# Optimization experiments

Measured on AMD Instinct MI355X. Metric: run time of the kernel, lower is better.

Reference implementation:

```python
import jax, jax.numpy as jnp
import numpy as np

N, D = 8192, 128
TEMPERATURE = 0.5


def _l2_normalize(x, eps):
    # matches F.normalize / utils.sim_matrix norm clamping
    n = jnp.linalg.norm(x, axis=1, keepdims=True)
    return x / jnp.maximum(n, eps)


def setup_inputs() -> dict:
    key = jax.random.key(0)
    k1, k2, k3 = jax.random.split(key, 3)
    nodes = jax.random.normal(k1, (N, D), dtype=jnp.float32)
    pair_nodes = jax.random.normal(k2, (N, D), dtype=jnp.float32)
    nodes_labels = jax.random.randint(k3, (N,), 0, 20).astype(jnp.int64)
    # standard NT-Xent self-mask: exclude diagonal from the denominator
    mask = jnp.eye(N, dtype=bool)
    return {"nodes": nodes, "pair_nodes": pair_nodes,
            "nodes_labels": nodes_labels, "mask": mask}


def reference(nodes, pair_nodes, nodes_labels, mask):
    # z, z_p: F.normalize(..., dim=1), eps=1e-12
    z = _l2_normalize(nodes, 1e-12)
    z_p = _l2_normalize(pair_nodes, 1e-12)
    # pairwise cosine similarity [N, N] == z @ z_p.T since rows are unit-norm
    positive_similarity = jnp.einsum('id,jd->ij', z, z_p)
    nominator = jnp.exp(positive_similarity / TEMPERATURE)  # [N, N]
    # utils.sim_matrix(nodes, nodes): cosine sim matrix with eps=1e-8 clamp
    zn = _l2_normalize(nodes, 1e-8)
    similarity_matrix = jnp.einsum('id,jd->ij', zn, zn)  # [N, N]
    denominator = (~mask).astype(jnp.float32) * jnp.exp(similarity_matrix / TEMPERATURE)
    den_sum = jnp.sum(denominator, axis=1)  # [N]
    # torch broadcasting: [N,N] / [N] divides along the LAST axis (columns)
    loss_partial = -jnp.log(nominator / den_sum[None, :])
    loss = jnp.sum(loss_partial) / nodes.shape[0]
    return loss
```

## Files before the change

kernel.cpp:

```cpp
#include <hip/hip_runtime.h>

#define N 8192
#define D 128
#define EXP_SCALE 2.8853900817779268f

typedef __bf16 bf16;
typedef __bf16 bf16x8 __attribute__((ext_vector_type(8)));
typedef float f32x4 __attribute__((ext_vector_type(4)));

#define ZBF_OFF 0
#define DEN_OFF (N * D * 2)
#define S_OFF   (DEN_OFF + N * 4)
#define SP_OFF  (S_OFF + 512)

__global__ __launch_bounds__(64) void norm_kernel(
    const float* __restrict__ nodes, const float* __restrict__ pair,
    bf16* __restrict__ zbf, float* __restrict__ svec, float* __restrict__ spvec)
{
    const int lane = threadIdx.x;
    const bool isPair = blockIdx.x >= 512;
    const float* src = isPair ? pair : nodes;
    const int row0 = (blockIdx.x & 511) * 16;

    float acc0 = 0.f, acc1 = 0.f;
    for (int rr = 0; rr < 16; ++rr) {
        const int row = row0 + rr;
        const float x0 = src[row * D + lane];
        const float x1 = src[row * D + lane + 64];
        float ss = x0 * x0 + x1 * x1;
        #pragma unroll
        for (int m = 32; m >= 1; m >>= 1) ss += __shfl_xor(ss, m, 64);
        const float nrm = sqrtf(ss);
        const float inv12 = 1.f / fmaxf(nrm, 1e-12f);
        acc0 += x0 * inv12;
        acc1 += x1 * inv12;
        if (!isPair) {
            const float inv8 = 1.f / fmaxf(nrm, 1e-8f);
            zbf[row * D + lane]      = (bf16)(x0 * inv8);
            zbf[row * D + lane + 64] = (bf16)(x1 * inv8);
        }
    }
    float* dst = isPair ? spvec : svec;
    atomicAdd(&dst[lane], acc0);
    atomicAdd(&dst[lane + 64], acc1);
}

#define LDP 80

__global__ __launch_bounds__(256) void gemm_kernel(
    const bf16* __restrict__ zbf, float* __restrict__ den)
{
    __shared__ bf16 As[128 * LDP];
    __shared__ bf16 Bs[128 * LDP];

    const int tid  = threadIdx.x;
    const int lane = tid & 63, wave = tid >> 6;
    const int wm = wave >> 1, wn = wave & 1;
    const int quad = lane >> 4, c = lane & 15;
    const int jbase = blockIdx.y * 128;
    const int kbase = blockIdx.x * 128;

    f32x4 acc[4][4];
    #pragma unroll
    for (int i = 0; i < 4; ++i)
        #pragma unroll
        for (int j = 0; j < 4; ++j) acc[i][j] = (f32x4){0.f, 0.f, 0.f, 0.f};

    #pragma unroll
    for (int kh = 0; kh < 2; ++kh) {
        __syncthreads();
        #pragma unroll
        for (int i = 0; i < 4; ++i) {
            const int chunk = tid + 256 * i;
            const int row = chunk >> 3;
            const int c8  = (chunk & 7) * 8;
            const uint4 va = *(const uint4*)(zbf + (jbase + row) * D + kh * 64 + c8);
            const uint4 vb = *(const uint4*)(zbf + (kbase + row) * D + kh * 64 + c8);
            *(uint4*)(&As[row * LDP + c8]) = va;
            *(uint4*)(&Bs[row * LDP + c8]) = vb;
        }
        __syncthreads();
        #pragma unroll
        for (int ks = 0; ks < 2; ++ks) {
            const int kk = ks * 32;
            bf16x8 af[4], bfr[4];
            #pragma unroll
            for (int mi = 0; mi < 4; ++mi)
                af[mi] = *(const bf16x8*)(&As[(wm * 64 + mi * 16 + c) * LDP + kk + quad * 8]);
            #pragma unroll
            for (int ni = 0; ni < 4; ++ni)
                bfr[ni] = *(const bf16x8*)(&Bs[(wn * 64 + ni * 16 + c) * LDP + kk + quad * 8]);
            #pragma unroll
            for (int mi = 0; mi < 4; ++mi)
                #pragma unroll
                for (int ni = 0; ni < 4; ++ni)
                    acc[mi][ni] = __builtin_amdgcn_mfma_f32_16x16x32_bf16(
                        af[mi], bfr[ni], acc[mi][ni], 0, 0, 0);
        }
    }

    #pragma unroll
    for (int mi = 0; mi < 4; ++mi) {
        const int growb = jbase + wm * 64 + mi * 16 + quad * 4;
        float rs[4] = {0.f, 0.f, 0.f, 0.f};
        #pragma unroll
        for (int ni = 0; ni < 4; ++ni) {
            const int gcol = kbase + wn * 64 + ni * 16 + c;
            const f32x4 cv = acc[mi][ni];
            #pragma unroll
            for (int r = 0; r < 4; ++r) {
                float e = __builtin_exp2f(cv[r] * EXP_SCALE);
                if (growb + r == gcol) e = 0.f;
                rs[r] += e;
            }
        }
        #pragma unroll
        for (int r = 0; r < 4; ++r) {
            #pragma unroll
            for (int m = 1; m <= 8; m <<= 1) rs[r] += __shfl_xor(rs[r], m, 64);
        }
        if (c == 0) {
            #pragma unroll
            for (int r = 0; r < 4; ++r) atomicAdd(&den[growb + r], rs[r]);
        }
    }
}

__global__ __launch_bounds__(256) void final_kernel(
    const float* __restrict__ den, const float* __restrict__ s,
    const float* __restrict__ sp, float* __restrict__ out)
{
    __shared__ float red[4];
    const int tid = threadIdx.x;
    float v = 0.f;
    for (int j = tid; j < N; j += 256) v += logf(den[j]);
    if (tid < 128) v -= s[tid] * sp[tid] * (1.f / 4096.f);
    #pragma unroll
    for (int m = 32; m >= 1; m >>= 1) v += __shfl_xor(v, m, 64);
    if ((tid & 63) == 0) red[tid >> 6] = v;
    __syncthreads();
    if (tid == 0) out[0] = red[0] + red[1] + red[2] + red[3];
}

extern "C" void kernel_launch(void* const* d_in, const int* in_sizes, int n_in,
                              void* d_out, int out_size, void* d_ws, size_t ws_size,
                              hipStream_t stream)
{
    const float* nodes = (const float*)d_in[0];
    const float* pair  = (const float*)d_in[1];

    char*  ws  = (char*)d_ws;
    bf16*  zbf = (bf16*)(ws + ZBF_OFF);
    float* den = (float*)(ws + DEN_OFF);
    float* s   = (float*)(ws + S_OFF);
    float* sp  = (float*)(ws + SP_OFF);

    hipMemsetAsync(ws + DEN_OFF, 0, N * 4 + 1024, stream);

    hipLaunchKernelGGL(norm_kernel, dim3(1024), dim3(64), 0, stream,
                       nodes, pair, zbf, s, sp);
    hipLaunchKernelGGL(gemm_kernel, dim3(64, 64), dim3(256), 0, stream, zbf, den);
    hipLaunchKernelGGL(final_kernel, dim3(1), dim3(256), 0, stream,
                       den, s, sp, (float*)d_out);
}
```

Measured before the change: 398.2 us.

## Exploit symmetry of self-similarity matrix with upper-triangular tile grid

The Gram matrix zn·znᵀ is symmetric, so the GEMM kernel now launches only the upper-triangular 128x128 tiles and adds each off-diagonal tile's exp values into both row and column denominators, with partial sums gathered in shared memory before the global atomics. This roughly halves the MFMA and exp work. It also switches to the hardware exp2 intrinsic, and the norm kernel now uses 256-thread blocks with float2 loads and a shared-memory reduction to cut global atomics. The cost is extra column-reduction shuffles, shared atomics and a per-block tile-index computation using double-precision sqrt.

```diff
diff --git a/kernel.cpp b/kernel.cpp
--- a/kernel.cpp
+++ b/kernel.cpp
@@ -2,9 +2,11 @@
 
 #define N 8192
 #define D 128
+#define NT 64
 #define EXP_SCALE 2.8853900817779268f
 
 typedef __bf16 bf16;
+typedef __bf16 bf16x2 __attribute__((ext_vector_type(2)));
 typedef __bf16 bf16x8 __attribute__((ext_vector_type(8)));
 typedef float f32x4 __attribute__((ext_vector_type(4)));
 
@@ -13,36 +15,43 @@
 #define S_OFF   (DEN_OFF + N * 4)
 #define SP_OFF  (S_OFF + 512)
 
-__global__ __launch_bounds__(64) void norm_kernel(
+__global__ __launch_bounds__(256) void norm_kernel(
     const float* __restrict__ nodes, const float* __restrict__ pair,
     bf16* __restrict__ zbf, float* __restrict__ svec, float* __restrict__ spvec)
 {
-    const int lane = threadIdx.x;
-    const bool isPair = blockIdx.x >= 512;
+    __shared__ float red[4][128];
+    const int tid = threadIdx.x;
+    const int lane = tid & 63, wave = tid >> 6;
+    const bool isPair = blockIdx.x >= 128;
     const float* src = isPair ? pair : nodes;
-    const int row0 = (blockIdx.x & 511) * 16;
+    const int row0 = (blockIdx.x & 127) * 64 + wave * 16;
 
     float acc0 = 0.f, acc1 = 0.f;
     for (int rr = 0; rr < 16; ++rr) {
         const int row = row0 + rr;
-        const float x0 = src[row * D + lane];
-        const float x1 = src[row * D + lane + 64];
-        float ss = x0 * x0 + x1 * x1;
+        const float2 x = *(const float2*)(src + row * D + lane * 2);
+        float ss = x.x * x.x + x.y * x.y;
         #pragma unroll
         for (int m = 32; m >= 1; m >>= 1) ss += __shfl_xor(ss, m, 64);
         const float nrm = sqrtf(ss);
         const float inv12 = 1.f / fmaxf(nrm, 1e-12f);
-        acc0 += x0 * inv12;
-        acc1 += x1 * inv12;
+        acc0 += x.x * inv12;
+        acc1 += x.y * inv12;
         if (!isPair) {
             const float inv8 = 1.f / fmaxf(nrm, 1e-8f);
-            zbf[row * D + lane]      = (bf16)(x0 * inv8);
-            zbf[row * D + lane + 64] = (bf16)(x1 * inv8);
-        }
-    }
-    float* dst = isPair ? spvec : svec;
-    atomicAdd(&dst[lane], acc0);
-    atomicAdd(&dst[lane + 64], acc1);
+            bf16x2 pk;
+            pk[0] = (bf16)(x.x * inv8);
+            pk[1] = (bf16)(x.y * inv8);
+            *(bf16x2*)(zbf + row * D + lane * 2) = pk;
+        }
+    }
+    red[wave][lane * 2]     = acc0;
+    red[wave][lane * 2 + 1] = acc1;
+    __syncthreads();
+    if (tid < 128) {
+        float* dst = isPair ? spvec : svec;
+        atomicAdd(&dst[tid], red[0][tid] + red[1][tid] + red[2][tid] + red[3][tid]);
+    }
 }
 
 #define LDP 80
@@ -52,13 +61,24 @@
 {
     __shared__ bf16 As[128 * LDP];
     __shared__ bf16 Bs[128 * LDP];
+    __shared__ float rowacc[128];
+    __shared__ float colacc[128];
+
+    int b = blockIdx.x;
+    int ti = (int)((2.0 * NT + 1.0 - sqrt((2.0 * NT + 1.0) * (2.0 * NT + 1.0) - 8.0 * (double)b)) * 0.5);
+    while (ti > 0 && ti * (2 * NT + 1 - ti) / 2 > b) --ti;
+    while ((ti + 1) * (2 * NT - ti) / 2 <= b) ++ti;
+    const int tj = ti + (b - ti * (2 * NT + 1 - ti) / 2);
+    const bool diag = (ti == tj);
 
     const int tid  = threadIdx.x;
     const int lane = tid & 63, wave = tid >> 6;
     const int wm = wave >> 1, wn = wave & 1;
     const int quad = lane >> 4, c = lane & 15;
-    const int jbase = blockIdx.y * 128;
-    const int kbase = blockIdx.x * 128;
+    const int ibase = ti * 128;
+    const int jbase = tj * 128;
+
+    if (tid < 128) { rowacc[tid] = 0.f; colacc[tid] = 0.f; }
 
     f32x4 acc[4][4];
     #pragma unroll
@@ -74,8 +94,8 @@
             const int chunk = tid + 256 * i;
             const int row = chunk >> 3;
             const int c8  = (chunk & 7) * 8;
-            const uint4 va = *(const uint4*)(zbf + (jbase + row) * D + kh * 64 + c8);
-            const uint4 vb = *(const uint4*)(zbf + (kbase + row) * D + kh * 64 + c8);
+            const uint4 va = *(const uint4*)(zbf + (ibase + row) * D + kh * 64 + c8);
+            const uint4 vb = *(const uint4*)(zbf + (jbase + row) * D + kh * 64 + c8);
             *(uint4*)(&As[row * LDP + c8]) = va;
             *(uint4*)(&Bs[row * LDP + c8]) = vb;
         }
@@ -99,30 +119,65 @@
         }
     }
 
+    float rowp[4][4];
+    float colp[4];
+    #pragma unroll
+    for (int mi = 0; mi < 4; ++mi)
+        #pragma unroll
+        for (int r = 0; r < 4; ++r) rowp[mi][r] = 0.f;
+    #pragma unroll
+    for (int ni = 0; ni < 4; ++ni) colp[ni] = 0.f;
+
     #pragma unroll
     for (int mi = 0; mi < 4; ++mi) {
-        const int growb = jbase + wm * 64 + mi * 16 + quad * 4;
-        float rs[4] = {0.f, 0.f, 0.f, 0.f};
+        const int lrow0 = wm * 64 + mi * 16 + quad * 4;
         #pragma unroll
         for (int ni = 0; ni < 4; ++ni) {
-            const int gcol = kbase + wn * 64 + ni * 16 + c;
+            const int lcol = wn * 64 + ni * 16 + c;
             const f32x4 cv = acc[mi][ni];
             #pragma unroll
             for (int r = 0; r < 4; ++r) {
-                float e = __builtin_exp2f(cv[r] * EXP_SCALE);
-                if (growb + r == gcol) e = 0.f;
-                rs[r] += e;
+                float e = __builtin_amdgcn_exp2f(cv[r] * EXP_SCALE);
+                if (diag && (lrow0 + r == lcol)) e = 0.f;
+                rowp[mi][r] += e;
+                colp[ni]    += e;
             }
         }
+    }
+
+    #pragma unroll
+    for (int mi = 0; mi < 4; ++mi)
         #pragma unroll
         for (int r = 0; r < 4; ++r) {
             #pragma unroll
-            for (int m = 1; m <= 8; m <<= 1) rs[r] += __shfl_xor(rs[r], m, 64);
-        }
-        if (c == 0) {
-            #pragma unroll
-            for (int r = 0; r < 4; ++r) atomicAdd(&den[growb + r], rs[r]);
-        }
+            for (int m = 1; m <= 8; m <<= 1)
+                rowp[mi][r] += __shfl_xor(rowp[mi][r], m, 64);
+        }
+    if (c == 0) {
+        #pragma unroll
+        for (int mi = 0; mi < 4; ++mi)
+            #pragma unroll
+            for (int r = 0; r < 4; ++r)
+                atomicAdd(&rowacc[wm * 64 + mi * 16 + quad * 4 + r], rowp[mi][r]);
+    }
+
+    if (!diag) {
+        #pragma unroll
+        for (int ni = 0; ni < 4; ++ni) {
+            colp[ni] += __shfl_xor(colp[ni], 16, 64);
+            colp[ni] += __shfl_xor(colp[ni], 32, 64);
+        }
+        if (quad == 0) {
+            #pragma unroll
+            for (int ni = 0; ni < 4; ++ni)
+                atomicAdd(&colacc[wn * 64 + ni * 16 + c], colp[ni]);
+        }
+    }
+
+    __syncthreads();
+    if (tid < 128) {
+        atomicAdd(&den[ibase + tid], rowacc[tid]);
+        if (!diag) atomicAdd(&den[jbase + tid], colacc[tid]);
     }
 }
 
@@ -157,9 +212,10 @@
 
     hipMemsetAsync(ws + DEN_OFF, 0, N * 4 + 1024, stream);
 
-    hipLaunchKernelGGL(norm_kernel, dim3(1024), dim3(64), 0, stream,
+    hipLaunchKernelGGL(norm_kernel, dim3(256), dim3(256), 0, stream,
                        nodes, pair, zbf, s, sp);
-    hipLaunchKernelGGL(gemm_kernel, dim3(64, 64), dim3(256), 0, stream, zbf, den);
+    hipLaunchKernelGGL(gemm_kernel, dim3(NT * (NT + 1) / 2), dim3(256), 0, stream,
+                       zbf, den);
     hipLaunchKernelGGL(final_kernel, dim3(1), dim3(256), 0, stream,
                        den, s, sp, (float*)d_out);
 }
```

Result: faster. 352.8 us (-11.4%).
